# Performance work log

Measured on AMD Instinct MI355X. Metric: run time of the kernel, lower is better.

Reference implementation:

```python
import jax, jax.numpy as jnp
import numpy as np

B, C, H, W = 8, 512, 32, 32
NUM_HEADS = 8
HEAD_DIM = C // NUM_HEADS


def setup_inputs() -> dict:
    key = jax.random.key(0)
    k1, k2, k3 = jax.random.split(key, 3)
    query = jax.random.normal(k1, (B, C, H, W), dtype=jnp.float32)
    key_value = jax.random.normal(k2, (B, C, H, W), dtype=jnp.float32)
    # Linear(dim, 3*dim): store as [C, 3C] so y = x @ W + b
    W_qkv = jax.random.normal(k3, (C, 3 * C), dtype=jnp.float32) * (C ** -0.5)
    b_qkv = jnp.zeros((3 * C,), dtype=jnp.float32)
    return {"query": query, "key_value": key_value, "W_qkv": W_qkv, "b_qkv": b_qkv}


def reference(query, key_value, W_qkv, b_qkv):
    Bb, Cc, Hh, Ww = query.shape
    seq = Hh * Ww
    scale = HEAD_DIM ** -0.5

    # [B, C, H, W] -> [B, S, C]
    q_seq = query.reshape(Bb, Cc, seq).transpose(0, 2, 1)
    kv_seq = key_value.reshape(Bb, Cc, seq).transpose(0, 2, 1)

    # Original calls full qkv_proj and slices; math == projecting with sliced weights.
    q = q_seq @ W_qkv[:, :Cc] + b_qkv[:Cc]
    k = kv_seq @ W_qkv[:, Cc:2 * Cc] + b_qkv[Cc:2 * Cc]
    v = kv_seq @ W_qkv[:, 2 * Cc:] + b_qkv[2 * Cc:]

    def heads(x):  # [B, S, C] -> [B, nH, S, hd]
        return x.reshape(Bb, seq, NUM_HEADS, HEAD_DIM).transpose(0, 2, 1, 3)

    q, k, v = heads(q), heads(k), heads(v)
    attn = jnp.einsum('bhqd,bhkd->bhqk', q, k) * scale
    attn = jax.nn.softmax(attn, axis=-1)  # dropout: identity in eval
    out = jnp.einsum('bhqk,bhkd->bhqd', attn, v)
    # [B, nH, S, hd] -> [B, S, C] -> [B, C, H, W]
    out = out.transpose(0, 2, 1, 3).reshape(Bb, seq, Cc)
    return out.transpose(0, 2, 1).reshape(Bb, Cc, Hh, Ww)
```

## Files before the change

kernel.cpp:

```cpp
#include <hip/hip_runtime.h>
#include <hip/hip_bf16.h>

using short4v = __attribute__((ext_vector_type(4))) short;
using short8  = __attribute__((ext_vector_type(8))) short;
using uint2v  = __attribute__((ext_vector_type(2))) unsigned int;
using f32x4   = __attribute__((ext_vector_type(4))) float;

static constexpr int CDIM = 512;
static constexpr float KSCALE = 0.125f * 1.44269504088896341f;

__device__ __forceinline__ short f2bf(float f) {
  unsigned u = __builtin_bit_cast(unsigned, f);
  u = (u + 0x7fffu + ((u >> 16) & 1u)) >> 16;
  return (short)(unsigned short)u;
}
__device__ __forceinline__ unsigned pack_bf16(float a, float b) {
  return (unsigned)(unsigned short)f2bf(a) | ((unsigned)(unsigned short)f2bf(b) << 16);
}

#define GLOAD_LDS16(gp, lp)                                                              \
  __builtin_amdgcn_global_load_lds((const __attribute__((address_space(1))) void*)(gp),  \
                                   (__attribute__((address_space(3))) void*)(lp), 16, 0, 0)
#define MFMA16(a, b, c) __builtin_amdgcn_mfma_f32_16x16x32_bf16((a), (b), (c), 0, 0, 0)

#define LDS_FENCE()                        \
  do {                                     \
    asm volatile("" ::: "memory");         \
    __builtin_amdgcn_s_waitcnt(0xc07f);    \
    __builtin_amdgcn_sched_barrier(0);     \
  } while (0)

__global__ __launch_bounds__(256) void prep_transpose(const float* __restrict__ query,
                                                      const float* __restrict__ keyv,
                                                      const float* __restrict__ Wqkv,
                                                      short* __restrict__ Xq_t,
                                                      short* __restrict__ Xkv_t,
                                                      short* __restrict__ W_t) {
  __shared__ float tile[64 * 65];
  const int id = blockIdx.x;
  const float* s; short* d; int R, C, r0, c0;
  if (id < 2048) {
    const int which = id >> 10;
    int rem = id & 1023;
    const int b = rem >> 7; rem &= 127;
    R = 512; C = 1024;
    s = (which ? keyv : query) + (size_t)b * 512 * 1024;
    d = (which ? Xkv_t : Xq_t) + (size_t)b * 512 * 1024;
    r0 = (rem >> 4) * 64; c0 = (rem & 15) * 64;
  } else {
    const int rem = id - 2048;
    R = 512; C = 1536; s = Wqkv; d = W_t;
    r0 = (rem / 24) * 64; c0 = (rem % 24) * 64;
  }
  const int t  = threadIdx.x;
  const int rr = t >> 4;
  const int c4 = (t & 15) * 4;
#pragma unroll
  for (int i = 0; i < 4; ++i) {
    const int r = rr + i * 16;
    f32x4 v = *(const f32x4*)(s + (size_t)(r0 + r) * C + c0 + c4);
#pragma unroll
    for (int j = 0; j < 4; ++j) tile[(c4 + j) * 65 + r] = v[j];
  }
  __syncthreads();
  const int r8 = (t & 7) * 8;
#pragma unroll
  for (int i = 0; i < 2; ++i) {
    const int c = (t >> 3) + i * 32;
    short8 pk;
#pragma unroll
    for (int j = 0; j < 8; ++j) pk[j] = f2bf(tile[c * 65 + r8 + j]);
    *(short8*)(d + (size_t)(c0 + c) * R + r0 + r8) = pk;
  }
}

__global__ __launch_bounds__(256, 2) void qkv_gemm(const short* __restrict__ Xq,
                                                   const short* __restrict__ Xkv,
                                                   const short* __restrict__ Wt,
                                                   const float* __restrict__ bias,
                                                   short* __restrict__ Qg,
                                                   short* __restrict__ Kg,
                                                   short* __restrict__ Vt) {
  __shared__ short Asm[128 * 64];
  __shared__ short Bsm[256 * 64];
  __shared__ short epi[4 * 1152];
  const int id = blockIdx.x;
  const int n_blk = id >> 6;
  const int m_blk = ((id & 7) << 3) | ((id >> 3) & 7);
  const int n0 = n_blk << 8;
  const int m0 = m_blk << 7;
  const short* A = (n0 < CDIM) ? Xq : Xkv;
  const int t = threadIdx.x;
  const int w = t >> 6, l = t & 63;
  const int wm = w & 1, wn = w >> 1;
  const int lc = l & 15, lr = l >> 4;

  f32x4 acc[4][8];
#pragma unroll
  for (int i = 0; i < 4; ++i)
#pragma unroll
    for (int j = 0; j < 8; ++j) acc[i][j] = (f32x4){0.f, 0.f, 0.f, 0.f};

  for (int kb = 0; kb < 8; ++kb) {
    const int k0 = kb * 64;
#pragma unroll
    for (int i = 0; i < 4; ++i) {
      const int Qi = (w * 4 + i) * 64 + l;
      const int row = Qi >> 3, u = Qi & 7;
      GLOAD_LDS16(A + (size_t)(m0 + row) * CDIM + k0 + ((u ^ (row & 7)) * 8), &Asm[Qi * 8]);
    }
#pragma unroll
    for (int i = 0; i < 8; ++i) {
      const int Qi = (w * 8 + i) * 64 + l;
      const int row = Qi >> 3, u = Qi & 7;
      GLOAD_LDS16(Wt + (size_t)(n0 + row) * CDIM + k0 + ((u ^ (row & 7)) * 8), &Bsm[Qi * 8]);
    }
    __syncthreads();
#pragma unroll
    for (int kc = 0; kc < 2; ++kc) {
      short8 af[4], bfr[8];
#pragma unroll
      for (int mt = 0; mt < 4; ++mt) {
        const int row = wm * 64 + mt * 16 + lc;
        af[mt] = *(const short8*)(&Asm[(row * 8 + ((kc * 4 + lr) ^ (row & 7))) * 8]);
      }
#pragma unroll
      for (int nt = 0; nt < 8; ++nt) {
        const int row = wn * 128 + nt * 16 + lc;
        bfr[nt] = *(const short8*)(&Bsm[(row * 8 + ((kc * 4 + lr) ^ (row & 7))) * 8]);
      }
#pragma unroll
      for (int mt = 0; mt < 4; ++mt)
#pragma unroll
        for (int nt = 0; nt < 8; ++nt)
          acc[mt][nt] = MFMA16(af[mt], bfr[nt], acc[mt][nt]);
    }
    __syncthreads();
  }

  const int M0 = m0 + wm * 64;
  const int bb = M0 >> 10, s0 = M0 & 1023;
  const int N0 = n0 + wn * 128;
  float bv[8];
#pragma unroll
  for (int nt = 0; nt < 8; ++nt) bv[nt] = bias[N0 + nt * 16 + lc];
  short* slab = epi + w * 1152;

#pragma unroll
  for (int hi = 0; hi < 2; ++hi) {
    const int hg = (N0 >> 6) + hi;
    const int part = hg >> 3, hh = hg & 7;
    const int nb = hi * 4;
    if (part < 2) {
      const float osc = part ? 1.f : KSCALE;
      short* obase = (part ? Kg : Qg) + (size_t)(bb * 8 + hh) * 65536 + (size_t)s0 * 64;
#pragma unroll
      for (int mt = 0; mt < 4; ++mt) {
#pragma unroll
        for (int ntL = 0; ntL < 4; ++ntL)
#pragma unroll
          for (int r = 0; r < 4; ++r)
            slab[(lr * 4 + r) * 72 + ntL * 16 + lc] =
                f2bf((acc[mt][nb + ntL][r] + bv[nb + ntL]) * osc);
        LDS_FENCE();
#pragma unroll
        for (int i = 0; i < 2; ++i) {
          const int slot = i * 64 + l;
          const int m_l = slot >> 3, n8 = (slot & 7) * 8;
          short8 vv = *(const short8*)(&slab[m_l * 72 + n8]);
          *(short8*)(obase + (size_t)(mt * 16 + m_l) * 64 + n8) = vv;
        }
        LDS_FENCE();
      }
    } else {
      short* vbase = Vt + (size_t)(bb * 8 + hh) * 65536;
#pragma unroll
      for (int ntL = 0; ntL < 4; ++ntL) {
#pragma unroll
        for (int mt = 0; mt < 4; ++mt)
#pragma unroll
          for (int r = 0; r < 4; ++r)
            slab[lc * 72 + mt * 16 + lr * 4 + r] = f2bf(acc[mt][nb + ntL][r] + bv[nb + ntL]);
        LDS_FENCE();
#pragma unroll
        for (int i = 0; i < 2; ++i) {
          const int slot = i * 64 + l;
          const int dloc = slot >> 3, ch = (slot & 7) * 8;
          short8 vv = *(const short8*)(&slab[dloc * 72 + ch]);
          *(short8*)(vbase + (size_t)(ntL * 16 + dloc) * 1024 + s0 + ch) = vv;
        }
        LDS_FENCE();
      }
    }
  }
}

__global__ __launch_bounds__(256, 2) void flash_attn(const short* __restrict__ Qg,
                                                     const short* __restrict__ Kg,
                                                     const short* __restrict__ Vt,
                                                     float* __restrict__ out) {
  __shared__ alignas(16) short smem[25600];
  short* Ksm = smem;
  short* Vsm = smem + 8192;
  const int bh = blockIdx.x;
  const int b = bh >> 3, h = bh & 7;
  const int q0 = blockIdx.y * 128;
  const int t = threadIdx.x;
  const int w = t >> 6, l = t & 63;
  const int quad = l >> 4, l15 = l & 15;
  short* Pw = smem + 16384 + w * 2304;

  const short* Qbase = Qg + (size_t)bh * 65536;
  const short* Kbase = Kg + (size_t)bh * 65536;
  const short* Vbase = Vt + (size_t)bh * 65536;

  short8 bq[2][2];
#pragma unroll
  for (int qs = 0; qs < 2; ++qs) {
    const short* qrow = Qbase + (size_t)(q0 + qs * 64 + w * 16 + l15) * 64;
    bq[qs][0] = *(const short8*)(qrow + quad * 8);
    bq[qs][1] = *(const short8*)(qrow + 32 + quad * 8);
  }

  float lp[2] = {0.f, 0.f};
  f32x4 Oac[2][4];
#pragma unroll
  for (int qs = 0; qs < 2; ++qs)
#pragma unroll
    for (int dt = 0; dt < 4; ++dt) Oac[qs][dt] = (f32x4){0.f, 0.f, 0.f, 0.f};

  for (int it2 = 0; it2 < 8; ++it2) {
#pragma unroll
    for (int half = 0; half < 2; ++half) {
      const int kk0 = (it2 * 2 + half) * 64;
      short* Kd = Ksm + half * 4096;
      short* Vd = Vsm + half * 4096;
#pragma unroll
      for (int i = 0; i < 2; ++i) {
        const int Qi = (w * 2 + i) * 64 + l;
        const int sr = Qi >> 3, u = Qi & 7;
        GLOAD_LDS16(Kbase + (size_t)(kk0 + sr) * 64 + (u ^ (sr & 7)) * 8, &Kd[Qi * 8]);
        GLOAD_LDS16(Vbase + (size_t)sr * 1024 + kk0 + (u ^ (sr & 7)) * 8, &Vd[Qi * 8]);
      }
    }
    __syncthreads();

#pragma unroll
    for (int half = 0; half < 2; ++half) {
      const short* Kh = Ksm + half * 4096;
      const short* Vh = Vsm + half * 4096;
      short8 kf[2][4];
#pragma unroll
      for (int c = 0; c < 2; ++c)
#pragma unroll
        for (int nt = 0; nt < 4; ++nt) {
          const int srow = nt * 16 + l15;
          kf[c][nt] = *(const short8*)(&Kh[(srow * 8 + ((c * 4 + quad) ^ (srow & 7))) * 8]);
        }

#pragma unroll
      for (int qs = 0; qs < 2; ++qs) {
        f32x4 st[4];
#pragma unroll
        for (int nt = 0; nt < 4; ++nt) {
          st[nt] = (f32x4){0.f, 0.f, 0.f, 0.f};
#pragma unroll
          for (int c = 0; c < 2; ++c) st[nt] = MFMA16(kf[c][nt], bq[qs][c], st[nt]);
        }
        short* Ps = Pw + qs * 1152;
#pragma unroll
        for (int nt = 0; nt < 4; ++nt) {
          float p0 = __builtin_amdgcn_exp2f(st[nt][0]);
          float p1 = __builtin_amdgcn_exp2f(st[nt][1]);
          float p2 = __builtin_amdgcn_exp2f(st[nt][2]);
          float p3 = __builtin_amdgcn_exp2f(st[nt][3]);
          lp[qs] += (p0 + p1) + (p2 + p3);
          uint2v pk;
          pk[0] = pack_bf16(p0, p1);
          pk[1] = pack_bf16(p2, p3);
          *(short4v*)(&Ps[l15 * 72 + (nt * 4 + quad) * 4]) = __builtin_bit_cast(short4v, pk);
        }
      }
      LDS_FENCE();

#pragma unroll
      for (int c = 0; c < 2; ++c) {
        short8 pb0 = *(const short8*)(&Pw[l15 * 72 + (c * 8 + quad * 2) * 4]);
        short8 pb1 = *(const short8*)(&Pw[1152 + l15 * 72 + (c * 8 + quad * 2) * 4]);
#pragma unroll
        for (int dt = 0; dt < 4; ++dt) {
          const int drow = dt * 16 + l15;
          short8 vf = *(const short8*)(&Vh[(drow * 8 + ((c * 4 + quad) ^ (drow & 7))) * 8]);
          Oac[0][dt] = MFMA16(vf, pb0, Oac[0][dt]);
          Oac[1][dt] = MFMA16(vf, pb1, Oac[1][dt]);
        }
      }
      __syncthreads();
    }
  }

#pragma unroll
  for (int qs = 0; qs < 2; ++qs) {
    float lv = lp[qs];
    lv += __shfl_xor(lv, 16, 64);
    lv += __shfl_xor(lv, 32, 64);
    const float rinv = 1.f / lv;
    float* ob = out + ((size_t)(b * 512 + h * 64)) * 1024 + q0 + qs * 64 + w * 16 + l15;
#pragma unroll
    for (int dt = 0; dt < 4; ++dt)
#pragma unroll
      for (int r = 0; r < 4; ++r)
        ob[(size_t)(dt * 16 + quad * 4 + r) * 1024] = Oac[qs][dt][r] * rinv;
  }
}

extern "C" void kernel_launch(void* const* d_in, const int* in_sizes, int n_in,
                              void* d_out, int out_size, void* d_ws, size_t ws_size,
                              hipStream_t stream) {
  const float* query = (const float*)d_in[0];
  const float* keyv  = (const float*)d_in[1];
  const float* Wqkv  = (const float*)d_in[2];
  const float* bqkv  = (const float*)d_in[3];
  float* out = (float*)d_out;
  short* ws  = (short*)d_ws;

  short* Xq_t  = ws;
  short* Xkv_t = ws + 4194304;
  short* W_t   = ws + 8388608;
  short* Qg    = ws + 9175040;
  short* Kg    = ws + 13369344;
  short* Vt    = ws + 17563648;

  prep_transpose<<<dim3(2240), 256, 0, stream>>>(query, keyv, Wqkv, Xq_t, Xkv_t, W_t);
  qkv_gemm<<<dim3(384), 256, 0, stream>>>(Xq_t, Xkv_t, W_t, bqkv, Qg, Kg, Vt);
  flash_attn<<<dim3(64, 8, 1), 256, 0, stream>>>(Qg, Kg, Vt, out);
}
```

Measured before the change: 131.6 us.

## Double-buffer K/V tiles with async prefetch and MFMA priority hints

Restructures the attention loop from load-two-tiles-then-compute into a double-buffered pipeline. The next 64-key K/V tile is prefetched into the alternate LDS buffer while the current one is computed, using a partial vmcnt wait plus barrier instead of a full __syncthreads. It also raises wave priority around the MFMA sections with s_setprio. The aim is to hide global-to-LDS load latency behind compute. The cost is an extra barrier per tile, and correctness depends on the hand-counted vmcnt(4).

```diff
diff --git a/kernel.cpp b/kernel.cpp
--- a/kernel.cpp
+++ b/kernel.cpp
@@ -28,6 +28,26 @@
     asm volatile("" ::: "memory");         \
     __builtin_amdgcn_s_waitcnt(0xc07f);    \
     __builtin_amdgcn_sched_barrier(0);     \
+  } while (0)
+
+#define TILE_SYNC(N)                                          \
+  do {                                                        \
+    __builtin_amdgcn_sched_barrier(0);                        \
+    asm volatile("s_waitcnt vmcnt(" #N ")" ::: "memory");     \
+    __builtin_amdgcn_sched_barrier(0);                        \
+    __builtin_amdgcn_s_barrier();                             \
+    asm volatile("" ::: "memory");                            \
+    __builtin_amdgcn_sched_barrier(0);                        \
+  } while (0)
+
+#define TILE_BAR()                                            \
+  do {                                                        \
+    __builtin_amdgcn_sched_barrier(0);                        \
+    asm volatile("s_waitcnt lgkmcnt(0)" ::: "memory");        \
+    __builtin_amdgcn_sched_barrier(0);                        \
+    __builtin_amdgcn_s_barrier();                             \
+    asm volatile("" ::: "memory");                            \
+    __builtin_amdgcn_sched_barrier(0);                        \
   } while (0)
 
 __global__ __launch_bounds__(256) void prep_transpose(const float* __restrict__ query,
@@ -229,74 +249,82 @@
 #pragma unroll
     for (int dt = 0; dt < 4; ++dt) Oac[qs][dt] = (f32x4){0.f, 0.f, 0.f, 0.f};
 
-  for (int it2 = 0; it2 < 8; ++it2) {
-#pragma unroll
-    for (int half = 0; half < 2; ++half) {
-      const int kk0 = (it2 * 2 + half) * 64;
-      short* Kd = Ksm + half * 4096;
-      short* Vd = Vsm + half * 4096;
-#pragma unroll
-      for (int i = 0; i < 2; ++i) {
-        const int Qi = (w * 2 + i) * 64 + l;
-        const int sr = Qi >> 3, u = Qi & 7;
-        GLOAD_LDS16(Kbase + (size_t)(kk0 + sr) * 64 + (u ^ (sr & 7)) * 8, &Kd[Qi * 8]);
-        GLOAD_LDS16(Vbase + (size_t)sr * 1024 + kk0 + (u ^ (sr & 7)) * 8, &Vd[Qi * 8]);
-      }
-    }
-    __syncthreads();
-
-#pragma unroll
-    for (int half = 0; half < 2; ++half) {
-      const short* Kh = Ksm + half * 4096;
-      const short* Vh = Vsm + half * 4096;
-      short8 kf[2][4];
-#pragma unroll
-      for (int c = 0; c < 2; ++c)
-#pragma unroll
-        for (int nt = 0; nt < 4; ++nt) {
-          const int srow = nt * 16 + l15;
-          kf[c][nt] = *(const short8*)(&Kh[(srow * 8 + ((c * 4 + quad) ^ (srow & 7))) * 8]);
-        }
-
-#pragma unroll
-      for (int qs = 0; qs < 2; ++qs) {
-        f32x4 st[4];
-#pragma unroll
-        for (int nt = 0; nt < 4; ++nt) {
-          st[nt] = (f32x4){0.f, 0.f, 0.f, 0.f};
-#pragma unroll
-          for (int c = 0; c < 2; ++c) st[nt] = MFMA16(kf[c][nt], bq[qs][c], st[nt]);
-        }
-        short* Ps = Pw + qs * 1152;
-#pragma unroll
-        for (int nt = 0; nt < 4; ++nt) {
-          float p0 = __builtin_amdgcn_exp2f(st[nt][0]);
-          float p1 = __builtin_amdgcn_exp2f(st[nt][1]);
-          float p2 = __builtin_amdgcn_exp2f(st[nt][2]);
-          float p3 = __builtin_amdgcn_exp2f(st[nt][3]);
-          lp[qs] += (p0 + p1) + (p2 + p3);
-          uint2v pk;
-          pk[0] = pack_bf16(p0, p1);
-          pk[1] = pack_bf16(p2, p3);
-          *(short4v*)(&Ps[l15 * 72 + (nt * 4 + quad) * 4]) = __builtin_bit_cast(short4v, pk);
-        }
-      }
-      LDS_FENCE();
-
-#pragma unroll
-      for (int c = 0; c < 2; ++c) {
-        short8 pb0 = *(const short8*)(&Pw[l15 * 72 + (c * 8 + quad * 2) * 4]);
-        short8 pb1 = *(const short8*)(&Pw[1152 + l15 * 72 + (c * 8 + quad * 2) * 4]);
-#pragma unroll
-        for (int dt = 0; dt < 4; ++dt) {
-          const int drow = dt * 16 + l15;
-          short8 vf = *(const short8*)(&Vh[(drow * 8 + ((c * 4 + quad) ^ (drow & 7))) * 8]);
-          Oac[0][dt] = MFMA16(vf, pb0, Oac[0][dt]);
-          Oac[1][dt] = MFMA16(vf, pb1, Oac[1][dt]);
-        }
-      }
-      __syncthreads();
-    }
+  auto stage_tile = [&](int tile, int buf) {
+    const int kk0 = tile * 64;
+    short* Kd = Ksm + buf * 4096;
+    short* Vd = Vsm + buf * 4096;
+#pragma unroll
+    for (int i = 0; i < 2; ++i) {
+      const int Qi = (w * 2 + i) * 64 + l;
+      const int sr = Qi >> 3, u = Qi & 7;
+      GLOAD_LDS16(Kbase + (size_t)(kk0 + sr) * 64 + (u ^ (sr & 7)) * 8, &Kd[Qi * 8]);
+      GLOAD_LDS16(Vbase + (size_t)sr * 1024 + kk0 + (u ^ (sr & 7)) * 8, &Vd[Qi * 8]);
+    }
+  };
+
+  stage_tile(0, 0);
+  for (int tt = 0; tt < 16; ++tt) {
+    const int buf = tt & 1;
+    if (tt < 15) {
+      stage_tile(tt + 1, buf ^ 1);
+      TILE_SYNC(4);
+    } else {
+      TILE_SYNC(0);
+    }
+
+    const short* Kh = Ksm + buf * 4096;
+    const short* Vh = Vsm + buf * 4096;
+    short8 kf[2][4];
+#pragma unroll
+    for (int c = 0; c < 2; ++c)
+#pragma unroll
+      for (int nt = 0; nt < 4; ++nt) {
+        const int srow = nt * 16 + l15;
+        kf[c][nt] = *(const short8*)(&Kh[(srow * 8 + ((c * 4 + quad) ^ (srow & 7))) * 8]);
+      }
+
+#pragma unroll
+    for (int qs = 0; qs < 2; ++qs) {
+      f32x4 st[4];
+      __builtin_amdgcn_s_setprio(1);
+#pragma unroll
+      for (int nt = 0; nt < 4; ++nt) {
+        st[nt] = (f32x4){0.f, 0.f, 0.f, 0.f};
+#pragma unroll
+        for (int c = 0; c < 2; ++c) st[nt] = MFMA16(kf[c][nt], bq[qs][c], st[nt]);
+      }
+      __builtin_amdgcn_s_setprio(0);
+      short* Ps = Pw + qs * 1152;
+#pragma unroll
+      for (int nt = 0; nt < 4; ++nt) {
+        float p0 = __builtin_amdgcn_exp2f(st[nt][0]);
+        float p1 = __builtin_amdgcn_exp2f(st[nt][1]);
+        float p2 = __builtin_amdgcn_exp2f(st[nt][2]);
+        float p3 = __builtin_amdgcn_exp2f(st[nt][3]);
+        lp[qs] += (p0 + p1) + (p2 + p3);
+        uint2v pk;
+        pk[0] = pack_bf16(p0, p1);
+        pk[1] = pack_bf16(p2, p3);
+        *(short4v*)(&Ps[l15 * 72 + (nt * 4 + quad) * 4]) = __builtin_bit_cast(short4v, pk);
+      }
+    }
+    LDS_FENCE();
+
+    __builtin_amdgcn_s_setprio(1);
+#pragma unroll
+    for (int c = 0; c < 2; ++c) {
+      short8 pb0 = *(const short8*)(&Pw[l15 * 72 + (c * 8 + quad * 2) * 4]);
+      short8 pb1 = *(const short8*)(&Pw[1152 + l15 * 72 + (c * 8 + quad * 2) * 4]);
+#pragma unroll
+      for (int dt = 0; dt < 4; ++dt) {
+        const int drow = dt * 16 + l15;
+        short8 vf = *(const short8*)(&Vh[(drow * 8 + ((c * 4 + quad) ^ (drow & 7))) * 8]);
+        Oac[0][dt] = MFMA16(vf, pb0, Oac[0][dt]);
+        Oac[1][dt] = MFMA16(vf, pb1, Oac[1][dt]);
+      }
+    }
+    __builtin_amdgcn_s_setprio(0);
+    TILE_BAR();
   }
 
 #pragma unroll
```

Measured after the change: 132.9 us. No clear change (+1.0%).
